# Performance work log

Hardware: AMD Instinct MI355X
Metric: run time of the kernel (lower is better)

Reference implementation:

```python
import jax, jax.numpy as jnp
import numpy as np
from jax import lax

TAU = 2.0
V_TH = 1.0
V_RESET = 0.0
SG_ALPHA = 4.0  # spikingjelly default Sigmoid surrogate
BN_EPS = 1e-5
KS = 8


@jax.custom_vjp
def heaviside(x):
    return (x >= 0.0).astype(x.dtype)

def _heaviside_fwd(x):
    return heaviside(x), x

def _heaviside_bwd(x, g):
    sg = jax.nn.sigmoid(SG_ALPHA * x)
    return (g * SG_ALPHA * sg * (1.0 - sg),)

heaviside.defvjp(_heaviside_fwd, _heaviside_bwd)


def lif_multistep(x_seq):
    # x_seq: [T, B, C, N]; hard reset, detach_reset=True, v_reset=0
    def step(v, x_t):
        v = v + (x_t - (v - V_RESET)) / TAU  # charge
        s = heaviside(v - V_TH)              # fire (surrogate grad)
        s_d = lax.stop_gradient(s)           # detach_reset
        v = (1.0 - s_d) * v + s_d * V_RESET  # hard reset
        return v, s
    v0 = jnp.zeros_like(x_seq[0])
    _, spikes = lax.scan(step, v0, x_seq)
    return spikes


def setup_inputs() -> dict:
    key = jax.random.key(0)
    k1, k2, k3 = jax.random.split(key, 3)
    T, B, C, N = 4, 32, 64, 4096
    Cout = 64
    x = jax.random.normal(k1, (T, B, C, N), dtype=jnp.float32)
    conv_w = jax.random.normal(k2, (Cout, C, KS), dtype=jnp.float32) * (1.0 / np.sqrt(C * KS))
    conv_b = jax.random.normal(k3, (Cout,), dtype=jnp.float32) * 0.01
    bn_gamma = jnp.ones((Cout,), dtype=jnp.float32)
    bn_beta = jnp.zeros((Cout,), dtype=jnp.float32)
    return {"x": x, "conv_w": conv_w, "conv_b": conv_b,
            "bn_gamma": bn_gamma, "bn_beta": bn_beta}


def reference(x, conv_w, conv_b, bn_gamma, bn_beta):
    T, B, C, N = x.shape
    x2 = x.reshape(T * B, C, N)
    # PyTorch 'same' padding for even kernel 8: left=3, right=4
    out = lax.conv_general_dilated(
        x2, conv_w, window_strides=(1,), padding=[(3, 4)],
        dimension_numbers=("NCH", "OIH", "NCH"))
    out = out + conv_b[None, :, None]
    # BatchNorm1d (training-mode batch stats over batch and length dims)
    mean = jnp.mean(out, axis=(0, 2), keepdims=True)
    var = jnp.mean(jnp.square(out - mean), axis=(0, 2), keepdims=True)
    out = (out - mean) * lax.rsqrt(var + BN_EPS)
    out = out * bn_gamma[None, :, None] + bn_beta[None, :, None]
    out = out.reshape(T, B, -1, N)
    return lif_multistep(out)
```

## Files before the change

### kernel.cpp

```cpp
#include <hip/hip_runtime.h>
#include <math.h>

#define T_    4
#define B_    32
#define C_    64
#define CO_   64
#define N_    4096
#define K_    8
#define PL_   3
#define TB_   128
#define TN_   256
#define NT_   16
#define NBLK_ 2048

__global__ __launch_bounds__(256, 2)
void conv_stats_kernel(const float* __restrict__ x, const float* __restrict__ w,
                       float* __restrict__ y, float* __restrict__ psum)
{
    __shared__ float xs[32][TN_ + 8];

    const int bx   = blockIdx.x;
    const int tb   = bx >> 4;
    const int n0   = (bx & 15) * TN_;
    const int tid  = threadIdx.x;
    const int lane = tid & 63;
    const int cg   = __builtin_amdgcn_readfirstlane(tid >> 6) * 16;
    const int noff = lane * 4;

    float acc[16][4];
#pragma unroll
    for (int i = 0; i < 16; ++i)
#pragma unroll
        for (int j = 0; j < 4; ++j) acc[i][j] = 0.0f;

    const float* xrow = x + (size_t)tb * C_ * N_;

    for (int cc = 0; cc < 2; ++cc) {
        __syncthreads();
        for (int idx = tid; idx < 32 * (TN_ + 7); idx += 256) {
            int ci = idx / (TN_ + 7);
            int i  = idx - ci * (TN_ + 7);
            int n  = n0 - PL_ + i;
            float v = 0.0f;
            if (n >= 0 && n < N_) v = xrow[(size_t)(cc * 32 + ci) * N_ + n];
            xs[ci][i] = v;
        }
        __syncthreads();

        for (int ci2 = 0; ci2 < 32; ++ci2) {
            const int ci = cc * 32 + ci2;
            const float4* xp = (const float4*)(&xs[ci2][noff]);
            float4 xa = xp[0], xb = xp[1], xc = xp[2];
            float xr[12] = {xa.x, xa.y, xa.z, xa.w,
                            xb.x, xb.y, xb.z, xb.w,
                            xc.x, xc.y, xc.z, xc.w};
            const float* wp = w + ((size_t)cg * C_ + ci) * K_;
#pragma unroll
            for (int coi = 0; coi < 16; ++coi) {
                const float* wq = wp + coi * (C_ * K_);
#pragma unroll
                for (int k = 0; k < K_; ++k) {
                    const float wk = wq[k];
#pragma unroll
                    for (int j = 0; j < 4; ++j)
                        acc[coi][j] = fmaf(wk, xr[k + j], acc[coi][j]);
                }
            }
        }
    }

    float* yrow = y + (size_t)tb * CO_ * N_;
    const int nbase = n0 + noff;
#pragma unroll
    for (int coi = 0; coi < 16; ++coi) {
        const int co = cg + coi;
        float4 v = make_float4(acc[coi][0], acc[coi][1], acc[coi][2], acc[coi][3]);
        *(float4*)(&yrow[(size_t)co * N_ + nbase]) = v;
        float s1 = (v.x + v.y) + (v.z + v.w);
        float s2 = (v.x * v.x + v.y * v.y) + (v.z * v.z + v.w * v.w);
#pragma unroll
        for (int off = 32; off > 0; off >>= 1) {
            s1 += __shfl_down(s1, off);
            s2 += __shfl_down(s2, off);
        }
        if (lane == 0) {
            psum[(size_t)(co * 2 + 0) * NBLK_ + bx] = s1;
            psum[(size_t)(co * 2 + 1) * NBLK_ + bx] = s2;
        }
    }
}

__global__ __launch_bounds__(256)
void stats_kernel(const float* __restrict__ psum,
                  const float* __restrict__ gamma, const float* __restrict__ beta,
                  float* __restrict__ ss)
{
    __shared__ double red[256];
    const int co  = blockIdx.x;
    const int tid = threadIdx.x;

    double s1 = 0.0, s2 = 0.0;
    for (int i = tid; i < NBLK_; i += 256) {
        s1 += (double)psum[(size_t)(co * 2 + 0) * NBLK_ + i];
        s2 += (double)psum[(size_t)(co * 2 + 1) * NBLK_ + i];
    }
    red[tid] = s1;
    __syncthreads();
    for (int st = 128; st > 0; st >>= 1) {
        if (tid < st) red[tid] += red[tid + st];
        __syncthreads();
    }
    const double S1 = red[0];
    __syncthreads();
    red[tid] = s2;
    __syncthreads();
    for (int st = 128; st > 0; st >>= 1) {
        if (tid < st) red[tid] += red[tid + st];
        __syncthreads();
    }
    const double S2 = red[0];

    if (tid == 0) {
        const double M    = (double)TB_ * (double)N_;
        const double mean = S1 / M;
        const double var  = S2 / M - mean * mean;
        const double inv  = 1.0 / sqrt(var + 1e-5);
        const double g    = (double)gamma[co];
        const float scale = (float)(g * inv);
        const float shift = (float)((double)beta[co] - mean * g * inv);
        ss[co * 2 + 0] = scale;
        ss[co * 2 + 1] = shift;
    }
}

__global__ __launch_bounds__(256)
void lif_kernel(const float* __restrict__ y, const float* __restrict__ ss,
                float* __restrict__ out)
{
    const int bx = blockIdx.x;
    const int c  = bx & 63;
    const int b  = bx >> 6;
    const float scale = ss[c * 2 + 0];
    const float shift = ss[c * 2 + 1];
    const size_t base = ((size_t)b * CO_ + c) * N_;
    const size_t tstr = (size_t)B_ * CO_ * N_;

    for (int n = threadIdx.x * 4; n < N_; n += 256 * 4) {
        float4 yv[4];
        yv[0] = *(const float4*)(y + base + 0 * tstr + n);
        yv[1] = *(const float4*)(y + base + 1 * tstr + n);
        yv[2] = *(const float4*)(y + base + 2 * tstr + n);
        yv[3] = *(const float4*)(y + base + 3 * tstr + n);

        float yin[4][4] = {{yv[0].x, yv[0].y, yv[0].z, yv[0].w},
                           {yv[1].x, yv[1].y, yv[1].z, yv[1].w},
                           {yv[2].x, yv[2].y, yv[2].z, yv[2].w},
                           {yv[3].x, yv[3].y, yv[3].z, yv[3].w}};
        float so[4][4];
#pragma unroll
        for (int e = 0; e < 4; ++e) {
            float v = 0.0f;
#pragma unroll
            for (int t = 0; t < 4; ++t) {
                const float yn = fmaf(yin[t][e], scale, shift);
                v = v + (yn - v) * 0.5f;
                const float s = (v >= 1.0f) ? 1.0f : 0.0f;
                so[t][e] = s;
                v = (s != 0.0f) ? 0.0f : v;
            }
        }
#pragma unroll
        for (int t = 0; t < 4; ++t) {
            float4 o = make_float4(so[t][0], so[t][1], so[t][2], so[t][3]);
            *(float4*)(out + base + (size_t)t * tstr + n) = o;
        }
    }
}

extern "C" void kernel_launch(void* const* d_in, const int* in_sizes, int n_in,
                              void* d_out, int out_size, void* d_ws, size_t ws_size,
                              hipStream_t stream)
{
    const float* x     = (const float*)d_in[0];
    const float* w     = (const float*)d_in[1];
    const float* gamma = (const float*)d_in[3];
    const float* beta  = (const float*)d_in[4];
    float* out = (float*)d_out;

    char* ws = (char*)d_ws;
    const size_t y_bytes    = (size_t)TB_ * CO_ * N_ * sizeof(float);
    const size_t psum_bytes = (size_t)CO_ * 2 * NBLK_ * sizeof(float);
    float* y    = (float*)ws;
    float* psum = (float*)(ws + y_bytes);
    float* ss   = (float*)(ws + y_bytes + psum_bytes);

    conv_stats_kernel<<<NBLK_, 256, 0, stream>>>(x, w, y, psum);
    stats_kernel<<<CO_, 256, 0, stream>>>(psum, gamma, beta, ss);
    lif_kernel<<<B_ * CO_, 256, 0, stream>>>(y, ss, out);
}
```

Before: 572.9 us.

## Use packed FMA over output-channel pairs with prepacked weights in conv

A small kernel interleaves the conv weights for adjacent output-channel pairs into float2 form. The conv inner loop then issues packed two-wide FMAs (v_pk_fma_f32) with a broadcast input, which halves the FMA instruction count and the scalar weight loads. The shared-memory channel chunk shrinks from 32 to 16 and the launch bounds ask for 4 blocks per SM instead of 2, aiming for higher occupancy. The trade-off is an extra kernel launch, twice as many sync/load phases, and extra register pressure under the tighter occupancy target.

```diff
diff --git a/kernel.cpp b/kernel.cpp
--- a/kernel.cpp
+++ b/kernel.cpp
@@ -12,58 +12,77 @@
 #define TN_   256
 #define NT_   16
 #define NBLK_ 2048
-
-__global__ __launch_bounds__(256, 2)
-void conv_stats_kernel(const float* __restrict__ x, const float* __restrict__ w,
+#define CCH_  16
+
+typedef float v2f __attribute__((ext_vector_type(2)));
+
+__global__ __launch_bounds__(256)
+void pack_w_kernel(const float* __restrict__ w, v2f* __restrict__ wpk)
+{
+    int i = blockIdx.x * 256 + threadIdx.x;
+    if (i < 32 * C_ * K_) {
+        int p = i >> 9;
+        int r = i & 511;
+        v2f v = { w[(size_t)(2 * p) * (C_ * K_) + r],
+                  w[(size_t)(2 * p + 1) * (C_ * K_) + r] };
+        wpk[i] = v;
+    }
+}
+
+__global__ __launch_bounds__(256, 4)
+void conv_stats_kernel(const float* __restrict__ x, const v2f* __restrict__ wpk,
                        float* __restrict__ y, float* __restrict__ psum)
 {
-    __shared__ float xs[32][TN_ + 8];
+    __shared__ float xs[CCH_][TN_ + 8];
 
     const int bx   = blockIdx.x;
     const int tb   = bx >> 4;
     const int n0   = (bx & 15) * TN_;
     const int tid  = threadIdx.x;
     const int lane = tid & 63;
-    const int cg   = __builtin_amdgcn_readfirstlane(tid >> 6) * 16;
+    const int wv   = __builtin_amdgcn_readfirstlane(tid >> 6);
+    const int cg   = wv * 16;
+    const int pg0  = wv * 8;
     const int noff = lane * 4;
 
-    float acc[16][4];
-#pragma unroll
-    for (int i = 0; i < 16; ++i)
-#pragma unroll
-        for (int j = 0; j < 4; ++j) acc[i][j] = 0.0f;
+    v2f acc[8][4];
+#pragma unroll
+    for (int p = 0; p < 8; ++p)
+#pragma unroll
+        for (int j = 0; j < 4; ++j) acc[p][j] = v2f{0.0f, 0.0f};
 
     const float* xrow = x + (size_t)tb * C_ * N_;
 
-    for (int cc = 0; cc < 2; ++cc) {
-        __syncthreads();
-        for (int idx = tid; idx < 32 * (TN_ + 7); idx += 256) {
+    for (int cc = 0; cc < C_ / CCH_; ++cc) {
+        __syncthreads();
+        for (int idx = tid; idx < CCH_ * (TN_ + 7); idx += 256) {
             int ci = idx / (TN_ + 7);
             int i  = idx - ci * (TN_ + 7);
             int n  = n0 - PL_ + i;
             float v = 0.0f;
-            if (n >= 0 && n < N_) v = xrow[(size_t)(cc * 32 + ci) * N_ + n];
+            if (n >= 0 && n < N_) v = xrow[(size_t)(cc * CCH_ + ci) * N_ + n];
             xs[ci][i] = v;
         }
         __syncthreads();
 
-        for (int ci2 = 0; ci2 < 32; ++ci2) {
-            const int ci = cc * 32 + ci2;
+        for (int ci2 = 0; ci2 < CCH_; ++ci2) {
+            const int ci = cc * CCH_ + ci2;
             const float4* xp = (const float4*)(&xs[ci2][noff]);
             float4 xa = xp[0], xb = xp[1], xc = xp[2];
             float xr[12] = {xa.x, xa.y, xa.z, xa.w,
                             xb.x, xb.y, xb.z, xb.w,
                             xc.x, xc.y, xc.z, xc.w};
-            const float* wp = w + ((size_t)cg * C_ + ci) * K_;
-#pragma unroll
-            for (int coi = 0; coi < 16; ++coi) {
-                const float* wq = wp + coi * (C_ * K_);
+#pragma unroll
+            for (int p = 0; p < 8; ++p) {
+                const v2f* wq = wpk + ((size_t)(pg0 + p) * C_ + ci) * K_;
 #pragma unroll
                 for (int k = 0; k < K_; ++k) {
-                    const float wk = wq[k];
-#pragma unroll
-                    for (int j = 0; j < 4; ++j)
-                        acc[coi][j] = fmaf(wk, xr[k + j], acc[coi][j]);
+                    const v2f wv2 = wq[k];
+#pragma unroll
+                    for (int j = 0; j < 4; ++j) {
+                        v2f xv = { xr[k + j], xr[k + j] };
+                        acc[p][j] = __builtin_elementwise_fma(wv2, xv, acc[p][j]);
+                    }
                 }
             }
         }
@@ -72,20 +91,26 @@
     float* yrow = y + (size_t)tb * CO_ * N_;
     const int nbase = n0 + noff;
 #pragma unroll
-    for (int coi = 0; coi < 16; ++coi) {
-        const int co = cg + coi;
-        float4 v = make_float4(acc[coi][0], acc[coi][1], acc[coi][2], acc[coi][3]);
-        *(float4*)(&yrow[(size_t)co * N_ + nbase]) = v;
-        float s1 = (v.x + v.y) + (v.z + v.w);
-        float s2 = (v.x * v.x + v.y * v.y) + (v.z * v.z + v.w * v.w);
-#pragma unroll
-        for (int off = 32; off > 0; off >>= 1) {
-            s1 += __shfl_down(s1, off);
-            s2 += __shfl_down(s2, off);
-        }
-        if (lane == 0) {
-            psum[(size_t)(co * 2 + 0) * NBLK_ + bx] = s1;
-            psum[(size_t)(co * 2 + 1) * NBLK_ + bx] = s2;
+    for (int p = 0; p < 8; ++p) {
+        const int co0 = cg + 2 * p;
+#pragma unroll
+        for (int h = 0; h < 2; ++h) {
+            float4 v;
+            if (h == 0) v = make_float4(acc[p][0].x, acc[p][1].x, acc[p][2].x, acc[p][3].x);
+            else        v = make_float4(acc[p][0].y, acc[p][1].y, acc[p][2].y, acc[p][3].y);
+            const int co = co0 + h;
+            *(float4*)(&yrow[(size_t)co * N_ + nbase]) = v;
+            float s1 = (v.x + v.y) + (v.z + v.w);
+            float s2 = (v.x * v.x + v.y * v.y) + (v.z * v.z + v.w * v.w);
+#pragma unroll
+            for (int off = 32; off > 0; off >>= 1) {
+                s1 += __shfl_down(s1, off);
+                s2 += __shfl_down(s2, off);
+            }
+            if (lane == 0) {
+                psum[(size_t)(co * 2 + 0) * NBLK_ + bx] = s1;
+                psum[(size_t)(co * 2 + 1) * NBLK_ + bx] = s2;
+            }
         }
     }
 }
@@ -193,8 +218,10 @@
     float* y    = (float*)ws;
     float* psum = (float*)(ws + y_bytes);
     float* ss   = (float*)(ws + y_bytes + psum_bytes);
-
-    conv_stats_kernel<<<NBLK_, 256, 0, stream>>>(x, w, y, psum);
+    v2f*   wpk  = (v2f*)(ws + y_bytes + psum_bytes + 512);
+
+    pack_w_kernel<<<64, 256, 0, stream>>>(w, wpk);
+    conv_stats_kernel<<<NBLK_, 256, 0, stream>>>(x, wpk, y, psum);
     stats_kernel<<<CO_, 256, 0, stream>>>(psum, gamma, beta, ss);
     lif_kernel<<<B_ * CO_, 256, 0, stream>>>(y, ss, out);
 }
```

After: 545.5 us. 4.8% less time.

## Register-prefetch conv input chunks, raise occupancy, fold BN stats into LIF kernel

Applied to the files above, without the earlier changes.

The conv kernel now stages 16-channel chunks of the input through registers. It prefetches the next chunk from global memory while computing on the current one in shared memory, and raises the launch-bounds occupancy hint from 2 to 4 blocks per CU. The separate stats kernel is removed, and each LIF block now redundantly reduces the per-channel partial sums in double precision before applying scale and shift. This cuts one launch and overlaps loads with FMAs, but each of the 2048 LIF blocks re-reads 16KB of psum, and the higher occupancy target may cause register spills given the 64 accumulators plus 17 prefetch registers.

```diff
diff --git a/kernel.cpp b/kernel.cpp
--- a/kernel.cpp
+++ b/kernel.cpp
@@ -12,12 +12,14 @@
 #define TN_   256
 #define NT_   16
 #define NBLK_ 2048
-
-__global__ __launch_bounds__(256, 2)
+#define CCH_  16
+#define ROWW_ (TN_ + 8)
+
+__global__ __launch_bounds__(256, 4)
 void conv_stats_kernel(const float* __restrict__ x, const float* __restrict__ w,
                        float* __restrict__ y, float* __restrict__ psum)
 {
-    __shared__ float xs[32][TN_ + 8];
+    __shared__ float xs[CCH_][ROWW_];
 
     const int bx   = blockIdx.x;
     const int tb   = bx >> 4;
@@ -27,6 +29,9 @@
     const int cg   = __builtin_amdgcn_readfirstlane(tid >> 6) * 16;
     const int noff = lane * 4;
 
+    const int ci_s = tid >> 4;
+    const int i0   = tid & 15;
+
     float acc[16][4];
 #pragma unroll
     for (int i = 0; i < 16; ++i)
@@ -35,20 +40,37 @@
 
     const float* xrow = x + (size_t)tb * C_ * N_;
 
-    for (int cc = 0; cc < 2; ++cc) {
-        __syncthreads();
-        for (int idx = tid; idx < 32 * (TN_ + 7); idx += 256) {
-            int ci = idx / (TN_ + 7);
-            int i  = idx - ci * (TN_ + 7);
-            int n  = n0 - PL_ + i;
-            float v = 0.0f;
-            if (n >= 0 && n < N_) v = xrow[(size_t)(cc * 32 + ci) * N_ + n];
-            xs[ci][i] = v;
-        }
-        __syncthreads();
-
-        for (int ci2 = 0; ci2 < 32; ++ci2) {
-            const int ci = cc * 32 + ci2;
+    float pf[17];
+#pragma unroll
+    for (int s = 0; s < 17; ++s) {
+        int i = i0 + 16 * s;
+        int n = n0 - PL_ + i;
+        float v = 0.0f;
+        if (i < TN_ + 7 && n >= 0 && n < N_) v = xrow[(size_t)ci_s * N_ + n];
+        pf[s] = v;
+    }
+#pragma unroll
+    for (int s = 0; s < 17; ++s) {
+        int i = i0 + 16 * s;
+        if (i < TN_ + 7) xs[ci_s][i] = pf[s];
+    }
+    __syncthreads();
+
+    for (int cc = 0; cc < C_ / CCH_; ++cc) {
+        if (cc < C_ / CCH_ - 1) {
+            const float* xnext = xrow + (size_t)(cc + 1) * CCH_ * N_;
+#pragma unroll
+            for (int s = 0; s < 17; ++s) {
+                int i = i0 + 16 * s;
+                int n = n0 - PL_ + i;
+                float v = 0.0f;
+                if (i < TN_ + 7 && n >= 0 && n < N_) v = xnext[(size_t)ci_s * N_ + n];
+                pf[s] = v;
+            }
+        }
+
+        for (int ci2 = 0; ci2 < CCH_; ++ci2) {
+            const int ci = cc * CCH_ + ci2;
             const float4* xp = (const float4*)(&xs[ci2][noff]);
             float4 xa = xp[0], xb = xp[1], xc = xp[2];
             float xr[12] = {xa.x, xa.y, xa.z, xa.w,
@@ -67,6 +89,16 @@
                 }
             }
         }
+
+        if (cc < C_ / CCH_ - 1) {
+            __syncthreads();
+#pragma unroll
+            for (int s = 0; s < 17; ++s) {
+                int i = i0 + 16 * s;
+                if (i < TN_ + 7) xs[ci_s][i] = pf[s];
+            }
+            __syncthreads();
+        }
     }
 
     float* yrow = y + (size_t)tb * CO_ * N_;
@@ -91,18 +123,22 @@
 }
 
 __global__ __launch_bounds__(256)
-void stats_kernel(const float* __restrict__ psum,
-                  const float* __restrict__ gamma, const float* __restrict__ beta,
-                  float* __restrict__ ss)
+void lif_kernel(const float* __restrict__ y, const float* __restrict__ psum,
+                const float* __restrict__ gamma, const float* __restrict__ beta,
+                float* __restrict__ out)
 {
     __shared__ double red[256];
-    const int co  = blockIdx.x;
+    __shared__ float ssf[2];
+
+    const int bx = blockIdx.x;
+    const int c  = bx & 63;
+    const int b  = bx >> 6;
     const int tid = threadIdx.x;
 
     double s1 = 0.0, s2 = 0.0;
     for (int i = tid; i < NBLK_; i += 256) {
-        s1 += (double)psum[(size_t)(co * 2 + 0) * NBLK_ + i];
-        s2 += (double)psum[(size_t)(co * 2 + 1) * NBLK_ + i];
+        s1 += (double)psum[(size_t)(c * 2 + 0) * NBLK_ + i];
+        s2 += (double)psum[(size_t)(c * 2 + 1) * NBLK_ + i];
     }
     red[tid] = s1;
     __syncthreads();
@@ -125,27 +161,18 @@
         const double mean = S1 / M;
         const double var  = S2 / M - mean * mean;
         const double inv  = 1.0 / sqrt(var + 1e-5);
-        const double g    = (double)gamma[co];
-        const float scale = (float)(g * inv);
-        const float shift = (float)((double)beta[co] - mean * g * inv);
-        ss[co * 2 + 0] = scale;
-        ss[co * 2 + 1] = shift;
-    }
-}
-
-__global__ __launch_bounds__(256)
-void lif_kernel(const float* __restrict__ y, const float* __restrict__ ss,
-                float* __restrict__ out)
-{
-    const int bx = blockIdx.x;
-    const int c  = bx & 63;
-    const int b  = bx >> 6;
-    const float scale = ss[c * 2 + 0];
-    const float shift = ss[c * 2 + 1];
+        const double g    = (double)gamma[c];
+        ssf[0] = (float)(g * inv);
+        ssf[1] = (float)((double)beta[c] - mean * g * inv);
+    }
+    __syncthreads();
+    const float scale = ssf[0];
+    const float shift = ssf[1];
+
     const size_t base = ((size_t)b * CO_ + c) * N_;
     const size_t tstr = (size_t)B_ * CO_ * N_;
 
-    for (int n = threadIdx.x * 4; n < N_; n += 256 * 4) {
+    for (int n = tid * 4; n < N_; n += 256 * 4) {
         float4 yv[4];
         yv[0] = *(const float4*)(y + base + 0 * tstr + n);
         yv[1] = *(const float4*)(y + base + 1 * tstr + n);
@@ -188,13 +215,10 @@
     float* out = (float*)d_out;
 
     char* ws = (char*)d_ws;
-    const size_t y_bytes    = (size_t)TB_ * CO_ * N_ * sizeof(float);
-    const size_t psum_bytes = (size_t)CO_ * 2 * NBLK_ * sizeof(float);
+    const size_t y_bytes = (size_t)TB_ * CO_ * N_ * sizeof(float);
     float* y    = (float*)ws;
     float* psum = (float*)(ws + y_bytes);
-    float* ss   = (float*)(ws + y_bytes + psum_bytes);
 
     conv_stats_kernel<<<NBLK_, 256, 0, stream>>>(x, w, y, psum);
-    stats_kernel<<<CO_, 256, 0, stream>>>(psum, gamma, beta, ss);
-    lif_kernel<<<B_ * CO_, 256, 0, stream>>>(y, ss, out);
+    lif_kernel<<<B_ * CO_, 256, 0, stream>>>(y, psum, gamma, beta, out);
 }
```

Measured after the change: 795.5 us. +38.8%, slower.
